# Performance work log

Hardware: AMD Instinct MI355X
Metric: run time of the kernel (lower is better)

## Reference

```python
import jax, jax.numpy as jnp
import numpy as np

NUM_GROUPS = 8   # num_groups1, recursive_index=False path
NUM_HEADS = 8


def setup_inputs() -> dict:
    key = jax.random.key(0)
    k1, k2, k3 = jax.random.split(key, 3)
    B, C, H, W = 4, 256, 64, 64
    x = jax.random.normal(k1, (B, C, H, W), dtype=jnp.float32)
    w_qkv = jax.random.normal(k2, (3 * C, C), dtype=jnp.float32) * 0.02
    w_proj = jax.random.normal(k3, (C, C), dtype=jnp.float32) * 0.02
    b_proj = jnp.zeros((C,), dtype=jnp.float32)
    return {"x": x, "w_qkv": w_qkv, "w_proj": w_proj, "b_proj": b_proj}


def reference(x, w_qkv, w_proj, b_proj):
    B, C, H, W = x.shape
    N = H * W
    G = NUM_GROUPS
    nh = NUM_HEADS
    hd = C // nh
    M = N // G
    scale = hd ** -0.5

    # b c h w -> b (h w) c
    xf = x.reshape(B, C, N).transpose(0, 2, 1)  # [B, N, C]

    # qkv linear (no bias), then split into groups / heads
    qkv = (xf @ w_qkv.T).reshape(B, G, M, 3, nh, hd)
    qkv = jnp.transpose(qkv, (3, 0, 1, 4, 2, 5))  # [3, B, G, nh, M, hd]
    q, k, v = qkv[0], qkv[1], qkv[2]

    # grouped multi-head attention, manual softmax
    attn = jax.nn.softmax(jnp.einsum('bghmd,bghnd->bghmn', q, k) * scale, axis=-1)
    out = jnp.einsum('bghmn,bghnd->bghmd', attn, v)

    # [B,G,nh,M,hd] -> [B,G,M,C] -> [B,N,C]
    out = out.transpose(0, 1, 3, 2, 4).reshape(B, N, C)

    out = out @ w_proj.T + b_proj

    # b (h w) c -> b c h w
    return out.transpose(0, 2, 1).reshape(B, C, H, W)
```

## Files before the change

kernel.cpp:

```cpp
#include <hip/hip_runtime.h>
#include <hip/hip_bf16.h>

#define Bb 4
#define Cc 256
#define Nn 4096
#define Gg 8
#define NHh 8
#define HDd 32
#define Mm 512

typedef __bf16 bf16_t;
typedef __bf16 bf16x2 __attribute__((ext_vector_type(2)));
typedef __bf16 bf16x4 __attribute__((ext_vector_type(4)));
typedef __bf16 bf16x8 __attribute__((ext_vector_type(8)));
typedef float f32x4 __attribute__((ext_vector_type(4)));

#define LSCALE (0.17677669529663687f * 1.44269504088896340f)

__device__ __forceinline__ void load_lds16(const bf16_t* g, bf16_t* l) {
  __builtin_amdgcn_global_load_lds(
      (const __attribute__((address_space(1))) void*)g,
      (__attribute__((address_space(3))) void*)l, 16, 0, 0);
}

__global__ __launch_bounds__(256) void prep_kernel(
    const float* __restrict__ x, bf16_t* __restrict__ xT,
    const float* __restrict__ wqkv, const float* __restrict__ wproj,
    bf16_t* __restrict__ wq_b, bf16_t* __restrict__ wp_b) {
  int bid = blockIdx.x, tid = threadIdx.x;
  if (bid >= 1024) {
    int i = (bid - 1024) * 256 + tid;
    wq_b[i] = (bf16_t)wqkv[i];
    if (i < Cc * Cc) wp_b[i] = (bf16_t)wproj[i];
    return;
  }
  __shared__ float t[64][65];
  int b = bid >> 8, c0 = ((bid >> 6) & 3) * 64, n0 = (bid & 63) * 64;
  const float* xp = x + ((long long)b * Cc + c0) * Nn + n0;
  for (int i = tid; i < 4096; i += 256) {
    int r = i >> 6, cc = i & 63;
    t[r][cc] = xp[(long long)r * Nn + cc];
  }
  __syncthreads();
  bf16_t* op = xT + ((long long)b * Nn + n0) * Cc + c0;
  for (int i = tid; i < 2048; i += 256) {
    int r = i >> 5, cc = (i & 31) * 2;
    bf16x2 w;
    w[0] = (bf16_t)t[cc][r];
    w[1] = (bf16_t)t[cc + 1][r];
    *(bf16x2*)&op[(long long)r * Cc + cc] = w;
  }
}

__global__ __launch_bounds__(256) void qkv_gemm_kernel(
    const bf16_t* __restrict__ xT, const bf16_t* __restrict__ wqb,
    bf16_t* __restrict__ Qh, bf16_t* __restrict__ Kh, bf16_t* __restrict__ Vh) {
  __shared__ bf16_t As[128 * 32];
  __shared__ bf16_t Bs[128 * 32];
  int bid = blockIdx.x;
  int tid = threadIdx.x, lane = tid & 63, wid = tid >> 6;
  int quad = lane >> 4, l16 = lane & 15;
  bool isQK = bid < 512;
  const bf16_t *A, *Bt;
  int m0, n0, z = 0;
  if (isQK) {
    m0 = (bid >> 2) * 128;
    n0 = (bid & 3) * 128;
    A = xT;
    Bt = wqb;
  } else {
    int vb = bid - 512;
    z = vb >> 6;
    int rem = vb & 63;
    m0 = (rem >> 5) * 128;
    n0 = (rem & 31) * 128;
    A = wqb + 512 * Cc;
    Bt = xT + (long long)z * Nn * Cc;
  }
  int wm = (wid >> 1) * 64, wn = (wid & 1) * 64;

  f32x4 acc[4][4];
#pragma unroll
  for (int i = 0; i < 4; ++i)
#pragma unroll
    for (int j = 0; j < 4; ++j) acc[i][j] = (f32x4){0.f, 0.f, 0.f, 0.f};

  int scol = (lane & 3) * 8;
  for (int k0 = 0; k0 < Cc; k0 += 32) {
    __syncthreads();
#pragma unroll
    for (int r = 0; r < 2; ++r) {
      int chunk = wid * 2 + r;
      int row = chunk * 16 + (lane >> 2);
      load_lds16(&A[(long long)(m0 + row) * Cc + k0 + scol], &As[chunk * 512]);
      load_lds16(&Bt[(long long)(n0 + row) * Cc + k0 + scol], &Bs[chunk * 512]);
    }
    __syncthreads();
    bf16x8 a[4], b[4];
#pragma unroll
    for (int i = 0; i < 4; ++i)
      a[i] = *(const bf16x8*)&As[(wm + i * 16 + l16) * 32 + quad * 8];
#pragma unroll
    for (int j = 0; j < 4; ++j)
      b[j] = *(const bf16x8*)&Bs[(wn + j * 16 + l16) * 32 + quad * 8];
#pragma unroll
    for (int i = 0; i < 4; ++i)
#pragma unroll
      for (int j = 0; j < 4; ++j)
        acc[i][j] = __builtin_amdgcn_mfma_f32_16x16x32_bf16(a[i], b[j], acc[i][j], 0, 0, 0);
  }

#pragma unroll
  for (int i = 0; i < 4; ++i) {
#pragma unroll
    for (int j = 0; j < 4; ++j) {
      int col = n0 + wn + j * 16 + l16;
#pragma unroll
      for (int r = 0; r < 4; ++r) {
        int row = m0 + wm + i * 16 + quad * 4 + r;
        float v = acc[i][j][r];
        if (isQK) {
          int bb = row >> 12, gg = (row >> 9) & 7, m = row & 511;
          int hh = (col >> 5) & 7, d = col & 31;
          long long hb = (long long)((bb << 6) | (gg << 3) | hh) * (Mm * HDd);
          if (col < 256)
            Qh[hb + m * HDd + d] = (bf16_t)(v * LSCALE);
          else
            Kh[hb + m * HDd + d] = (bf16_t)v;
        } else {
          int hh = row >> 5, d = row & 31, gg = col >> 9, m = col & 511;
          long long hb = (long long)((z << 6) | (gg << 3) | hh) * (Mm * HDd);
          Vh[hb + d * Mm + m] = (bf16_t)v;
        }
      }
    }
  }
}

__global__ __launch_bounds__(256, 2) void attn_kernel(
    const bf16_t* __restrict__ Qh, const bf16_t* __restrict__ Kh,
    const bf16_t* __restrict__ Vh, bf16_t* __restrict__ Oa) {
  __shared__ bf16_t Vs[32 * 520];
  int gid = blockIdx.x;
  int ms = gid & 1, head = gid >> 1;
  int h = head & 7, g = (head >> 3) & 7, b = head >> 6;
  int tid = threadIdx.x, lane = tid & 63, wid = tid >> 6;
  int quad = lane >> 4, l16 = lane & 15;

  const bf16_t* Kg = Kh + (long long)head * (Mm * HDd);
  const bf16_t* Vg = Vh + (long long)head * (Mm * HDd);
  const bf16_t* Qg = Qh + (long long)head * (Mm * HDd) + ms * 256 * HDd;

#pragma unroll
  for (int it = 0; it < 8; ++it) {
    int d = wid * 8 + it;
    load_lds16(&Vg[d * Mm + lane * 8], &Vs[d * 520]);
  }
  __syncthreads();

  int rp0 = ((l16 >> 2) << 3) | (l16 & 3);
  const bf16_t* Kp0 = Kg + rp0 * HDd + quad * 8;
  const bf16_t* Kp1 = Kp0 + 4 * HDd;
  const bf16_t* VsL = &Vs[l16 * 520 + quad * 8];
  const bf16_t* VsH = &Vs[(16 + l16) * 520 + quad * 8];
  const f32x4 zero = (f32x4){0.f, 0.f, 0.f, 0.f};

#pragma unroll 1
  for (int t = 0; t < 2; ++t) {
    int m0 = wid * 64 + t * 32;
    bf16x8 qa = *(const bf16x8*)&Qg[(m0 + l16) * HDd + quad * 8];
    bf16x8 qb = *(const bf16x8*)&Qg[(m0 + 16 + l16) * HDd + quad * 8];

    float sma = 0.f, smb = 0.f;
    f32x4 oLa = zero, oHa = zero, oLb = zero, oHb = zero;

#pragma unroll 4
    for (int c = 0; c < 16; ++c) {
      int nb = c * 32;
      bf16x8 kf0 = *(const bf16x8*)&Kp0[nb * HDd];
      bf16x8 kf1 = *(const bf16x8*)&Kp1[nb * HDd];
      f32x4 sa0 = __builtin_amdgcn_mfma_f32_16x16x32_bf16(kf0, qa, zero, 0, 0, 0);
      f32x4 sa1 = __builtin_amdgcn_mfma_f32_16x16x32_bf16(kf1, qa, zero, 0, 0, 0);
      f32x4 sb0 = __builtin_amdgcn_mfma_f32_16x16x32_bf16(kf0, qb, zero, 0, 0, 0);
      f32x4 sb1 = __builtin_amdgcn_mfma_f32_16x16x32_bf16(kf1, qb, zero, 0, 0, 0);
      bf16x8 pa, pb;
#pragma unroll
      for (int r = 0; r < 4; ++r) {
        float e0 = __builtin_exp2f(sa0[r]);
        float e1 = __builtin_exp2f(sa1[r]);
        sma += e0 + e1;
        pa[r] = (bf16_t)e0;
        pa[4 + r] = (bf16_t)e1;
        float f0 = __builtin_exp2f(sb0[r]);
        float f1 = __builtin_exp2f(sb1[r]);
        smb += f0 + f1;
        pb[r] = (bf16_t)f0;
        pb[4 + r] = (bf16_t)f1;
      }
      bf16x8 vL = *(const bf16x8*)&VsL[nb];
      bf16x8 vH = *(const bf16x8*)&VsH[nb];
      oLa = __builtin_amdgcn_mfma_f32_16x16x32_bf16(vL, pa, oLa, 0, 0, 0);
      oHa = __builtin_amdgcn_mfma_f32_16x16x32_bf16(vH, pa, oHa, 0, 0, 0);
      oLb = __builtin_amdgcn_mfma_f32_16x16x32_bf16(vL, pb, oLb, 0, 0, 0);
      oHb = __builtin_amdgcn_mfma_f32_16x16x32_bf16(vH, pb, oHb, 0, 0, 0);
    }

    sma += __shfl_xor(sma, 16, 64);
    sma += __shfl_xor(sma, 32, 64);
    smb += __shfl_xor(smb, 16, 64);
    smb += __shfl_xor(smb, 32, 64);
    float inva = 1.f / sma, invb = 1.f / smb;

    long long orowa =
        ((long long)(b * Nn + g * Mm + ms * 256 + m0 + l16)) * Cc + h * HDd;
    long long orowb = orowa + 16 * Cc;
    bf16x4 wLa, wHa, wLb, wHb;
#pragma unroll
    for (int r = 0; r < 4; ++r) {
      wLa[r] = (bf16_t)(oLa[r] * inva);
      wHa[r] = (bf16_t)(oHa[r] * inva);
      wLb[r] = (bf16_t)(oLb[r] * invb);
      wHb[r] = (bf16_t)(oHb[r] * invb);
    }
    *(bf16x4*)&Oa[orowa + quad * 4] = wLa;
    *(bf16x4*)&Oa[orowa + 16 + quad * 4] = wHa;
    *(bf16x4*)&Oa[orowb + quad * 4] = wLb;
    *(bf16x4*)&Oa[orowb + 16 + quad * 4] = wHb;
  }
}

__global__ __launch_bounds__(256) void proj_kernel(
    const bf16_t* __restrict__ Wp, const bf16_t* __restrict__ Oa,
    float* __restrict__ out, const float* __restrict__ bias) {
  __shared__ bf16_t As[128 * 32];
  __shared__ bf16_t Bs[128 * 32];
  int tid = threadIdx.x, lane = tid & 63, wid = tid >> 6;
  int quad = lane >> 4, l16 = lane & 15;
  int z = blockIdx.z;
  const bf16_t* Bt = Oa + (long long)z * Nn * Cc;
  int m0 = blockIdx.y * 128, n0 = blockIdx.x * 128;
  int wm = (wid >> 1) * 64, wn = (wid & 1) * 64;

  f32x4 acc[4][4];
#pragma unroll
  for (int i = 0; i < 4; ++i)
#pragma unroll
    for (int j = 0; j < 4; ++j) acc[i][j] = (f32x4){0.f, 0.f, 0.f, 0.f};

  int scol = (lane & 3) * 8;
  for (int k0 = 0; k0 < Cc; k0 += 32) {
    __syncthreads();
#pragma unroll
    for (int r = 0; r < 2; ++r) {
      int chunk = wid * 2 + r;
      int row = chunk * 16 + (lane >> 2);
      load_lds16(&Wp[(long long)(m0 + row) * Cc + k0 + scol], &As[chunk * 512]);
      load_lds16(&Bt[(long long)(n0 + row) * Cc + k0 + scol], &Bs[chunk * 512]);
    }
    __syncthreads();
    bf16x8 a[4], b[4];
#pragma unroll
    for (int i = 0; i < 4; ++i)
      a[i] = *(const bf16x8*)&As[(wm + i * 16 + l16) * 32 + quad * 8];
#pragma unroll
    for (int j = 0; j < 4; ++j)
      b[j] = *(const bf16x8*)&Bs[(wn + j * 16 + l16) * 32 + quad * 8];
#pragma unroll
    for (int i = 0; i < 4; ++i)
#pragma unroll
      for (int j = 0; j < 4; ++j)
        acc[i][j] = __builtin_amdgcn_mfma_f32_16x16x32_bf16(a[i], b[j], acc[i][j], 0, 0, 0);
  }

#pragma unroll
  for (int i = 0; i < 4; ++i) {
#pragma unroll
    for (int j = 0; j < 4; ++j) {
      int col = n0 + wn + j * 16 + l16;
#pragma unroll
      for (int r = 0; r < 4; ++r) {
        int row = m0 + wm + i * 16 + quad * 4 + r;
        out[(long long)z * (Cc * Nn) + (long long)row * Nn + col] =
            acc[i][j][r] + bias[row];
      }
    }
  }
}

extern "C" void kernel_launch(void* const* d_in, const int* in_sizes, int n_in,
                              void* d_out, int out_size, void* d_ws, size_t ws_size,
                              hipStream_t stream) {
  (void)in_sizes; (void)n_in; (void)out_size; (void)ws_size;
  const float* x = (const float*)d_in[0];
  const float* w_qkv = (const float*)d_in[1];
  const float* w_proj = (const float*)d_in[2];
  const float* b_proj = (const float*)d_in[3];
  float* out = (float*)d_out;

  char* ws = (char*)d_ws;
  bf16_t* xT  = (bf16_t*)(ws);
  bf16_t* wqb = (bf16_t*)(ws + 8388608);
  bf16_t* wpb = (bf16_t*)(ws + 8781824);
  bf16_t* Qh  = (bf16_t*)(ws + 8912896);
  bf16_t* Kh  = (bf16_t*)(ws + 17301504);
  bf16_t* Vh  = (bf16_t*)(ws + 25690112);
  bf16_t* Oa  = (bf16_t*)(ws + 34078720);

  prep_kernel<<<1792, 256, 0, stream>>>(x, xT, w_qkv, w_proj, wqb, wpb);
  qkv_gemm_kernel<<<768, 256, 0, stream>>>(xT, wqb, Qh, Kh, Vh);
  attn_kernel<<<512, 256, 0, stream>>>(Qh, Kh, Vh, Oa);
  proj_kernel<<<dim3(32, 2, 4), 256, 0, stream>>>(wpb, Oa, out, b_proj);
}
```

Before: 131.0 us.

## Stage K tile in LDS for attention and vectorize prep transpose

```diff
diff --git a/kernel.cpp b/kernel.cpp
--- a/kernel.cpp
+++ b/kernel.cpp
@@ -37,18 +37,26 @@
   __shared__ float t[64][65];
   int b = bid >> 8, c0 = ((bid >> 6) & 3) * 64, n0 = (bid & 63) * 64;
   const float* xp = x + ((long long)b * Cc + c0) * Nn + n0;
-  for (int i = tid; i < 4096; i += 256) {
-    int r = i >> 6, cc = i & 63;
-    t[r][cc] = xp[(long long)r * Nn + cc];
+#pragma unroll
+  for (int it = 0; it < 4; ++it) {
+    int idx = it * 256 + tid;
+    int r = idx >> 4, col = (idx & 15) * 4;
+    f32x4 v = *(const f32x4*)&xp[(long long)r * Nn + col];
+    t[r][col] = v[0];
+    t[r][col + 1] = v[1];
+    t[r][col + 2] = v[2];
+    t[r][col + 3] = v[3];
   }
   __syncthreads();
   bf16_t* op = xT + ((long long)b * Nn + n0) * Cc + c0;
-  for (int i = tid; i < 2048; i += 256) {
-    int r = i >> 5, cc = (i & 31) * 2;
-    bf16x2 w;
-    w[0] = (bf16_t)t[cc][r];
-    w[1] = (bf16_t)t[cc + 1][r];
-    *(bf16x2*)&op[(long long)r * Cc + cc] = w;
+#pragma unroll
+  for (int it = 0; it < 2; ++it) {
+    int idx = it * 256 + tid;
+    int n = idx >> 3, cg = (idx & 7) * 8;
+    bf16x8 w;
+#pragma unroll
+    for (int j = 0; j < 8; ++j) w[j] = (bf16_t)t[cg + j][n];
+    *(bf16x8*)&op[(long long)n * Cc + cg] = w;
   }
 }
 
@@ -140,6 +148,7 @@
 __global__ __launch_bounds__(256, 2) void attn_kernel(
     const bf16_t* __restrict__ Qh, const bf16_t* __restrict__ Kh,
     const bf16_t* __restrict__ Vh, bf16_t* __restrict__ Oa) {
+  __shared__ bf16_t Ks[512 * 32];
   __shared__ bf16_t Vs[32 * 520];
   int gid = blockIdx.x;
   int ms = gid & 1, head = gid >> 1;
@@ -153,13 +162,18 @@
 
 #pragma unroll
   for (int it = 0; it < 8; ++it) {
+    int chunk = wid * 8 + it;
+    load_lds16(&Kg[chunk * 512 + lane * 8], &Ks[chunk * 512]);
+  }
+#pragma unroll
+  for (int it = 0; it < 8; ++it) {
     int d = wid * 8 + it;
     load_lds16(&Vg[d * Mm + lane * 8], &Vs[d * 520]);
   }
   __syncthreads();
 
   int rp0 = ((l16 >> 2) << 3) | (l16 & 3);
-  const bf16_t* Kp0 = Kg + rp0 * HDd + quad * 8;
+  const bf16_t* Kp0 = &Ks[rp0 * HDd + quad * 8];
   const bf16_t* Kp1 = Kp0 + 4 * HDd;
   const bf16_t* VsL = &Vs[l16 * 520 + quad * 8];
   const bf16_t* VsH = &Vs[(16 + l16) * 520 + quad * 8];
```

Measured after the change: 124.2 us. 1.05x faster.
